# Kernel optimization log

Measured on AMD Instinct MI355X. Metric: run time of the kernel, lower is better.

Reference implementation:

```python
import jax, jax.numpy as jnp
import numpy as np

B, N, DEG = 64, 2048, 8
EPG = N * DEG            # edges per graph
E = B * EPG              # 1,048,576 total edges
NTOT = B * N             # 131,072 total nodes
HID = 128
NCLS = 32
K1 = int(np.ceil(0.25 * N))    # 512
K2 = int(np.ceil(0.25 * K1))   # 128


def _gcn(x, W, b, src, dst, emask, n):
    h = x @ W
    deg = jnp.zeros((n,), x.dtype).at[dst].add(emask) + 1.0
    dinv = jax.lax.rsqrt(deg)
    norm = dinv[src] * dinv[dst] * emask          # [E]
    agg = jnp.zeros((n, h.shape[1]), x.dtype).at[dst].add(h[src] * norm[:, None])
    agg = agg + h * (1.0 / deg)[:, None]          # self-loop term (norm = 1/deg)
    return agg + b


def _pool_stage(h, score, src, dst, emask, n_per_graph, k):
    # SAGPool top-k per graph (uniform graph size -> static k)
    sb = score.reshape(B, n_per_graph)
    idx = jax.lax.top_k(sb, k)[1]                                   # [B,k]
    perm = (jnp.arange(B)[:, None] * n_per_graph + idx).reshape(-1)  # [B*k]
    xp = h[perm] * jnp.tanh(score[perm])[:, None]
    # filter_adj: remap surviving nodes, mask dropped edges
    nmap = jnp.full((B * n_per_graph,), -1, jnp.int32).at[perm].set(
        jnp.arange(B * k, dtype=jnp.int32))
    s2, d2 = nmap[src], nmap[dst]
    m2 = emask * ((s2 >= 0) & (d2 >= 0)).astype(h.dtype)
    return xp, jnp.maximum(s2, 0), jnp.maximum(d2, 0), m2, perm


def _readout(x, k):
    xr = x.reshape(B, k, HID)
    return jnp.concatenate([xr.max(axis=1), xr.mean(axis=1)], axis=1)  # [B,2H]


def setup_inputs() -> dict:
    key = jax.random.key(0)
    ks = jax.random.split(key, 20)
    off = jnp.repeat(jnp.arange(B, dtype=jnp.int32) * N, EPG)
    src = jax.random.randint(ks[0], (E,), 0, N, dtype=jnp.int32) + off
    dst = jax.random.randint(ks[1], (E,), 0, N, dtype=jnp.int32) + off
    x = jax.random.normal(ks[2], (NTOT, 1), jnp.float32)
    ginfo = jax.random.normal(ks[3], (B, 10), jnp.float32)

    def lin(k, fi, fo):
        return jax.random.normal(k, (fi, fo), jnp.float32) / np.sqrt(fi)

    return {
        'x': x, 'edge_src': src, 'edge_dst': dst, 'ginfo': ginfo,
        'W1': lin(ks[4], 1, HID), 'b1': jnp.zeros((HID,), jnp.float32),
        'sW1': lin(ks[5], HID, 1), 'sb1': jnp.zeros((1,), jnp.float32),
        'W2': lin(ks[6], HID, HID), 'b2': jnp.zeros((HID,), jnp.float32),
        'sW2': lin(ks[7], HID, 1), 'sb2': jnp.zeros((1,), jnp.float32),
        'l1W': lin(ks[8], 2 * HID + 10, HID), 'l1b': jnp.zeros((HID,), jnp.float32),
        'l2W': lin(ks[9], HID, HID // 2), 'l2b': jnp.zeros((HID // 2,), jnp.float32),
        'l3W': lin(ks[10], HID // 2, NCLS), 'l3b': jnp.zeros((NCLS,), jnp.float32),
    }


def reference(x, edge_src, edge_dst, ginfo, W1, b1, sW1, sb1, W2, b2, sW2, sb2,
              l1W, l1b, l2W, l2b, l3W, l3b):
    m0 = jnp.ones((E,), x.dtype)
    # stage 1
    h = jax.nn.relu(_gcn(x, W1, b1, edge_src, edge_dst, m0, NTOT))
    score = _gcn(h, sW1, sb1, edge_src, edge_dst, m0, NTOT)[:, 0]
    h, s1, d1, m1, _ = _pool_stage(h, score, edge_src, edge_dst, m0, N, K1)
    x1 = _readout(h, K1)
    # stage 2
    n1 = B * K1
    h = jax.nn.relu(_gcn(h, W2, b2, s1, d1, m1, n1))
    score = _gcn(h, sW2, sb2, s1, d1, m1, n1)[:, 0]
    h, _, _, _, _ = _pool_stage(h, score, s1, d1, m1, K1, K2)
    x2 = _readout(h, K2)
    # head (dropout is eval-mode identity)
    z = jnp.concatenate([x1 + x2, ginfo.reshape(B, -1)], axis=1)
    z = jax.nn.relu(z @ l1W + l1b)
    z = jax.nn.relu(z @ l2W + l2b)
    return jax.nn.log_softmax(z @ l3W + l3b, axis=-1)
```

## Files before the change

kernel.cpp:

```cpp
#include <hip/hip_runtime.h>
#include <math.h>

#define NB    64
#define NPG   2048
#define EPG   16384
#define HID   128
#define K1V   512
#define K2V   128
#define N1    32768
#define MSK   (NPG - 1)
#define NQ    4
#define ESEG  (EPG / NQ)
#define SLOTS 24

typedef unsigned int u32;

static __device__ __forceinline__ float frelu(float v) { return v > 0.f ? v : 0.f; }

static __device__ __forceinline__ u32 f2key(float f) {
    u32 u = __float_as_uint(f);
    return u ^ ((u >> 31) ? 0xFFFFFFFFu : 0x80000000u);
}

static __device__ __forceinline__ u32 wave_iscan(u32 v, int lane) {
    #pragma unroll
    for (int off = 1; off < 64; off <<= 1) {
        u32 t = __shfl_up(v, off);
        if (lane >= off) v += t;
    }
    return v;
}

template <int N, int T>
static __device__ __forceinline__ void radix_top(const u32* __restrict__ key, int K,
                                                 u32* hist, u32* misc,
                                                 u32& tau, int& R) {
    const int tid = threadIdx.x;
    if (tid == 0) { misc[0] = 0u; misc[1] = (u32)K; }
    __syncthreads();
    #pragma unroll
    for (int p = 0; p < 4; p++) {
        const int shift = 24 - 8 * p;
        for (int i = tid; i < 256; i += T) hist[i] = 0u;
        __syncthreads();
        const u32 prefix = misc[0];
        const u32 need   = misc[1];
        for (int i = tid; i < N; i += T) {
            u32 k = key[i];
            bool ok = (p == 0) || ((k >> (shift + 8)) == prefix);
            if (ok) atomicAdd(&hist[(k >> shift) & 255u], 1u);
        }
        __syncthreads();
        if (tid < 64) {
            const int lane = tid;
            u32 c0 = hist[4 * lane + 0], c1 = hist[4 * lane + 1];
            u32 c2 = hist[4 * lane + 2], c3 = hist[4 * lane + 3];
            u32 local = c0 + c1 + c2 + c3;
            u32 inc = local;
            #pragma unroll
            for (int off = 1; off < 64; off <<= 1) {
                u32 v = __shfl_down(inc, off);
                if (lane + off < 64) inc += v;
            }
            u32 excl = inc - local;
            u32 ge3 = excl + c3, ge2 = ge3 + c2, ge1 = ge2 + c1, ge0 = ge1 + c0;
            int selb = -1; u32 gt = 0;
            if      (ge3 >= need && excl < need) { selb = 4 * lane + 3; gt = excl; }
            else if (ge2 >= need && ge3  < need) { selb = 4 * lane + 2; gt = ge3; }
            else if (ge1 >= need && ge2  < need) { selb = 4 * lane + 1; gt = ge2; }
            else if (ge0 >= need && ge1  < need) { selb = 4 * lane + 0; gt = ge1; }
            if (selb >= 0) { misc[0] = (prefix << 8) | (u32)selb; misc[1] = need - gt; }
        }
        __syncthreads();
    }
    tau = misc[0];
    R = (int)misc[1];
}

__global__ __launch_bounds__(1024) void k_sweepA(const float* __restrict__ x,
                                                 const int* __restrict__ esrc,
                                                 const int* __restrict__ edst,
                                                 float* __restrict__ df_g,
                                                 float* __restrict__ di_g,
                                                 float* __restrict__ tp) {
    __shared__ int   cnt[NPG];
    __shared__ float lv[NPG];
    __shared__ float acc[NPG];
    const int bid = blockIdx.x, tid = threadIdx.x;
    const int g = bid & 63, q = bid >> 6;
    for (int i = tid; i < NPG; i += 1024) { cnt[i] = 0; acc[i] = 0.f; }
    __syncthreads();
    const int4* dall = (const int4*)(edst + (size_t)g * EPG);
    for (int i = tid; i < EPG / 4; i += 1024) {
        int4 dd = dall[i];
        atomicAdd(&cnt[dd.x & MSK], 1); atomicAdd(&cnt[dd.y & MSK], 1);
        atomicAdd(&cnt[dd.z & MSK], 1); atomicAdd(&cnt[dd.w & MSK], 1);
    }
    __syncthreads();
    for (int i = tid; i < NPG; i += 1024) {
        float df = (float)cnt[i] + 1.0f;
        float di = rsqrtf(df);
        lv[i] = di * x[(size_t)g * NPG + i];
        if (q == 0) { df_g[(size_t)g * NPG + i] = df; di_g[(size_t)g * NPG + i] = di; }
    }
    __syncthreads();
    const int4* s4 = (const int4*)(esrc + g * EPG + q * ESEG);
    const int4* d4 = (const int4*)(edst + g * EPG + q * ESEG);
    for (int i = tid; i < ESEG / 4; i += 1024) {
        int4 ss = s4[i]; int4 dd = d4[i];
        atomicAdd(&acc[dd.x & MSK], lv[ss.x & MSK]);
        atomicAdd(&acc[dd.y & MSK], lv[ss.y & MSK]);
        atomicAdd(&acc[dd.z & MSK], lv[ss.z & MSK]);
        atomicAdd(&acc[dd.w & MSK], lv[ss.w & MSK]);
    }
    __syncthreads();
    float4* op = (float4*)(tp + ((size_t)g * NQ + q) * NPG);
    const float4* ap = (const float4*)acc;
    for (int i = tid; i < NPG / 4; i += 1024) op[i] = ap[i];
}

__global__ __launch_bounds__(1024) void k_sweepB(const float* __restrict__ x,
                                                 const int* __restrict__ esrc,
                                                 const int* __restrict__ edst,
                                                 const float* __restrict__ tp,
                                                 const float* __restrict__ df_g,
                                                 const float* __restrict__ di_g,
                                                 const float* __restrict__ W1,
                                                 const float* __restrict__ b1,
                                                 const float* __restrict__ sW1,
                                                 const float* __restrict__ sb1,
                                                 float* __restrict__ u_g,
                                                 float* __restrict__ sci_g,
                                                 float* __restrict__ scp) {
    __shared__ float lv[NPG];
    __shared__ float acc[NPG];
    __shared__ float lw[HID], lbb[HID], lsw[HID];
    const int bid = blockIdx.x, tid = threadIdx.x;
    const int g = bid & 63, q = bid >> 6;
    if (tid < HID) { lw[tid] = W1[tid]; lbb[tid] = b1[tid]; lsw[tid] = sW1[tid]; }
    __syncthreads();
    const float sb1v = sb1[0];
    for (int i = tid; i < NPG; i += 1024) {
        float t = 0.f;
        #pragma unroll
        for (int q2 = 0; q2 < NQ; q2++) t += tp[((size_t)g * NQ + q2) * NPG + i];
        float df = df_g[(size_t)g * NPG + i];
        float di = di_g[(size_t)g * NPG + i];
        float u = t * di + x[(size_t)g * NPG + i] / df;
        float s = 0.f;
        #pragma unroll 8
        for (int c = 0; c < HID; c++) s += frelu(fmaf(lw[c], u, lbb[c])) * lsw[c];
        lv[i] = di * s;
        acc[i] = 0.f;
        if (q == 0) {
            u_g[(size_t)g * NPG + i] = u;
            sci_g[(size_t)g * NPG + i] = s / df + sb1v;
        }
    }
    __syncthreads();
    const int4* s4 = (const int4*)(esrc + g * EPG + q * ESEG);
    const int4* d4 = (const int4*)(edst + g * EPG + q * ESEG);
    for (int i = tid; i < ESEG / 4; i += 1024) {
        int4 ss = s4[i]; int4 dd = d4[i];
        atomicAdd(&acc[dd.x & MSK], lv[ss.x & MSK]);
        atomicAdd(&acc[dd.y & MSK], lv[ss.y & MSK]);
        atomicAdd(&acc[dd.z & MSK], lv[ss.z & MSK]);
        atomicAdd(&acc[dd.w & MSK], lv[ss.w & MSK]);
    }
    __syncthreads();
    float4* op = (float4*)(scp + ((size_t)g * NQ + q) * NPG);
    const float4* ap = (const float4*)acc;
    for (int i = tid; i < NPG / 4; i += 1024) op[i] = ap[i];
}

__global__ __launch_bounds__(1024) void k_select(
    const float* __restrict__ sci_g, const float* __restrict__ di_g,
    const float* __restrict__ scp, const float* __restrict__ u_g,
    const float* __restrict__ W1, const float* __restrict__ b1,
    float* __restrict__ ulist, float* __restrict__ tg1, float* __restrict__ x1b,
    int* __restrict__ nmap_g, int* __restrict__ gdeg)
{
    __shared__ float lsc[NPG];
    __shared__ u32   lkey[NPG];
    __shared__ int   ln[NPG];
    __shared__ float ul[K1V], tgl[K1V];
    __shared__ int   sellist[K1V];
    __shared__ u32   hist[256], misc[2], wsum[16];
    __shared__ int   scnt;
    __shared__ float lw[HID], lbb[HID];
    const int b = blockIdx.x, tid = threadIdx.x;
    const int lane = tid & 63, wv = tid >> 6;

    if (tid < K1V) gdeg[b * K1V + tid] = 0;
    for (int i = tid; i < NPG; i += 1024) {
        float a = 0.f;
        #pragma unroll
        for (int q = 0; q < NQ; q++) a += scp[((size_t)b * NQ + q) * NPG + i];
        float sc = sci_g[(size_t)b * NPG + i] + di_g[(size_t)b * NPG + i] * a;
        lsc[i] = sc;
        lkey[i] = f2key(sc);
        ln[i] = -1;
    }
    if (tid < HID) { lw[tid] = W1[tid]; lbb[tid] = b1[tid]; }
    if (tid == 0) scnt = 0;
    __syncthreads();

    u32 tau; int R;
    radix_top<NPG, 1024>(lkey, K1V, hist, misc, tau, R);

    {
        int e0 = tid * 2, e1 = e0 + 1;
        u32 k0 = lkey[e0], k1 = lkey[e1];
        int q0 = (k0 == tau) ? 1 : 0, q1 = (k1 == tau) ? 1 : 0;
        u32 inc = wave_iscan((u32)(q0 + q1), lane);
        if (lane == 63) wsum[wv] = inc;
        __syncthreads();
        if (tid == 0) { u32 run = 0; for (int w2 = 0; w2 < 16; w2++) { u32 v = wsum[w2]; wsum[w2] = run; run += v; } }
        __syncthreads();
        u32 base = wsum[wv] + inc - (u32)(q0 + q1);
        bool sel0 = (k0 > tau) || (q0 && base < (u32)R);
        bool sel1 = (k1 > tau) || (q1 && (base + (u32)q0) < (u32)R);
        if (sel0) { int pos = atomicAdd(&scnt, 1); sellist[pos] = e0; }
        if (sel1) { int pos = atomicAdd(&scnt, 1); sellist[pos] = e1; }
        __syncthreads();
    }

    if (tid < K1V) {
        int node = sellist[tid];
        float uu = u_g[(size_t)b * NPG + node];
        float g = tanhf(lsc[node]);
        ul[tid] = uu; tgl[tid] = g;
        ulist[b * K1V + tid] = uu;
        tg1[b * K1V + tid] = g;
        ln[node] = tid;
    }
    __syncthreads();
    for (int i = tid; i < NPG; i += 1024) nmap_g[(size_t)b * NPG + i] = ln[i];

    float* rp = (float*)lkey;
    {
        int grp = tid >> 7, c = tid & 127;
        float w = lw[c], bb = lbb[c];
        float mx = -INFINITY, sm = 0.f;
        for (int j = grp; j < K1V; j += 8) {
            float v = frelu(fmaf(w, ul[j], bb)) * tgl[j];
            mx = fmaxf(mx, v); sm += v;
        }
        __syncthreads();
        rp[tid] = mx; rp[1024 + tid] = sm;
        __syncthreads();
        if (tid < HID) {
            float m2 = -INFINITY, s2 = 0.f;
            #pragma unroll
            for (int g2 = 0; g2 < 8; g2++) {
                m2 = fmaxf(m2, rp[g2 * 128 + tid]);
                s2 += rp[1024 + g2 * 128 + tid];
            }
            x1b[b * 256 + tid] = m2;
            x1b[b * 256 + HID + tid] = s2 / (float)K1V;
        }
    }
}

__global__ __launch_bounds__(512) void k_cpmm(
    const int* __restrict__ esrc, const int* __restrict__ edst,
    const int* __restrict__ nmap_g,
    int* __restrict__ gdeg, int* __restrict__ srcs2,
    const float* __restrict__ ulist, const float* __restrict__ tg1,
    const float* __restrict__ W1, const float* __restrict__ b1,
    const float* __restrict__ W2, float* __restrict__ hw)
{
    __shared__ union U {
        int lnm[NPG];
        struct { float lhT[HID * 64]; float lu[64]; float lg[64]; } mm;
    } sm;
    const int bid = blockIdx.x, tid = threadIdx.x;

    if (bid < NB * NQ) {
        const int g = bid & 63, q = bid >> 6;
        for (int i = tid; i < NPG; i += 512) sm.lnm[i] = nmap_g[(size_t)g * NPG + i];
        __syncthreads();
        const int4* s4 = (const int4*)(esrc + g * EPG + q * ESEG);
        const int4* d4 = (const int4*)(edst + g * EPG + q * ESEG);
        const int base = g * K1V;
        for (int i = tid; i < ESEG / 4; i += 512) {
            int4 ss = s4[i]; int4 dd = d4[i];
            int sa[4] = { ss.x & MSK, ss.y & MSK, ss.z & MSK, ss.w & MSK };
            int da[4] = { dd.x & MSK, dd.y & MSK, dd.z & MSK, dd.w & MSK };
            #pragma unroll
            for (int r = 0; r < 4; r++) {
                int s2 = sm.lnm[sa[r]], d2 = sm.lnm[da[r]];
                if (s2 >= 0 && d2 >= 0) {
                    int n = base + d2;
                    int slot = atomicAdd(&gdeg[n], 1);
                    if (slot < SLOTS) srcs2[(size_t)n * SLOTS + slot] = base + s2;
                }
            }
        }
    } else {
        const int row0 = (bid - NB * NQ) * 64;
        if (tid < 64) { sm.mm.lu[tid] = ulist[row0 + tid]; sm.mm.lg[tid] = tg1[row0 + tid]; }
        __syncthreads();
        for (int idx = tid; idx < HID * 64; idx += 512) {
            int k = idx >> 6, j = idx & 63;
            sm.mm.lhT[idx] = frelu(fmaf(W1[k], sm.mm.lu[j], b1[k])) * sm.mm.lg[j];
        }
        __syncthreads();
        const int cg2 = tid & 31, rg2 = tid >> 5;
        float acc[4][4];
        #pragma unroll
        for (int r = 0; r < 4; r++)
            #pragma unroll
            for (int c = 0; c < 4; c++) acc[r][c] = 0.f;
        const float4* lhT4 = (const float4*)sm.mm.lhT;
        #pragma unroll 4
        for (int k = 0; k < HID; k++) {
            float4 h = lhT4[k * 16 + rg2];
            float4 ww = *(const float4*)&W2[(size_t)k * HID + cg2 * 4];
            float hr[4] = { h.x, h.y, h.z, h.w };
            float wc[4] = { ww.x, ww.y, ww.z, ww.w };
            #pragma unroll
            for (int r = 0; r < 4; r++)
                #pragma unroll
                for (int c = 0; c < 4; c++)
                    acc[r][c] = fmaf(hr[r], wc[c], acc[r][c]);
        }
        #pragma unroll
        for (int r = 0; r < 4; r++) {
            float4 o; o.x = acc[r][0]; o.y = acc[r][1]; o.z = acc[r][2]; o.w = acc[r][3];
            *(float4*)&hw[(size_t)(row0 + rg2 * 4 + r) * HID + cg2 * 4] = o;
        }
    }
}

__global__ __launch_bounds__(256) void k_pull2(
    const int* __restrict__ srcs2, const int* __restrict__ gdeg,
    const float* __restrict__ hw, const float* __restrict__ b2,
    const float* __restrict__ sW2, const float* __restrict__ sb2,
    float* __restrict__ h2, float* __restrict__ ds02, float* __restrict__ sc2i)
{
    int node = blockIdx.x * 4 + (threadIdx.x >> 6);
    int lane = threadIdx.x & 63;
    int dg = gdeg[node];
    int cnt = dg < SLOTS ? dg : SLOTS;
    float a0 = 0.f, a1 = 0.f;
    for (int j = 0; j < cnt; j++) {
        int s = srcs2[(size_t)node * SLOTS + j];
        float w = rsqrtf((float)gdeg[s] + 1.0f);
        a0 = fmaf(w, hw[(size_t)s * HID + lane], a0);
        a1 = fmaf(w, hw[(size_t)s * HID + 64 + lane], a1);
    }
    float df = (float)dg + 1.0f;
    float di = rsqrtf(df);
    float h0 = frelu(a0 * di + hw[(size_t)node * HID + lane] / df + b2[lane]);
    float h1 = frelu(a1 * di + hw[(size_t)node * HID + 64 + lane] / df + b2[lane + 64]);
    h2[(size_t)node * HID + lane] = h0;
    h2[(size_t)node * HID + 64 + lane] = h1;
    float dot = h0 * sW2[lane] + h1 * sW2[lane + 64];
    #pragma unroll
    for (int o = 32; o > 0; o >>= 1) dot += __shfl_down(dot, o);
    if (lane == 0) {
        ds02[node] = di * dot;
        sc2i[node] = dot / df + sb2[0];
    }
}

__global__ __launch_bounds__(1024) void k_tkhead(
    const int* __restrict__ srcs2, const int* __restrict__ gdeg,
    const float* __restrict__ ds02, const float* __restrict__ sc2i,
    const float* __restrict__ h2,
    const float* __restrict__ x1b, const float* __restrict__ gi,
    const float* __restrict__ l1W, const float* __restrict__ l1b,
    const float* __restrict__ l2W, const float* __restrict__ l2b,
    const float* __restrict__ l3W, const float* __restrict__ l3b,
    float* __restrict__ out)
{
    __shared__ float sv[K1V];
    __shared__ u32   skey[K1V];
    __shared__ u32   hist[256], misc[2], wsum[16];
    __shared__ int   plist[K2V];
    __shared__ float tl[K2V];
    __shared__ float rp[1024], rp2[1024];
    __shared__ float z[272];
    __shared__ float zp[8][128];
    __shared__ float z1[HID], z2[64], z3[32], red[2];
    __shared__ int   scnt;
    const int b = blockIdx.x, tid = threadIdx.x;
    const int lane = tid & 63, wv = tid >> 6;
    if (tid == 0) scnt = 0;

    if (tid < K1V) {
        int n = b * K1V + tid;
        int dg = gdeg[n];
        int cnt = dg < SLOTS ? dg : SLOTS;
        float acc = 0.f;
        for (int j = 0; j < cnt; j++) acc += ds02[srcs2[(size_t)n * SLOTS + j]];
        float sc = sc2i[n] + rsqrtf((float)dg + 1.0f) * acc;
        sv[tid] = sc; skey[tid] = f2key(sc);
    }
    __syncthreads();
    u32 tau; int R;
    radix_top<K1V, 1024>(skey, K2V, hist, misc, tau, R);

    {
        u32 k0 = skey[tid < K1V ? tid : 0];
        int q0 = (tid < K1V && k0 == tau) ? 1 : 0;
        u32 inc = wave_iscan((u32)q0, lane);
        if (lane == 63) wsum[wv] = inc;
        __syncthreads();
        if (tid == 0) { u32 run = 0; for (int w2 = 0; w2 < 16; w2++) { u32 v = wsum[w2]; wsum[w2] = run; run += v; } }
        __syncthreads();
        u32 base = wsum[wv] + inc - (u32)q0;
        bool sel = (tid < K1V) && ((k0 > tau) || (q0 && base < (u32)R));
        if (sel) { int pos = atomicAdd(&scnt, 1); plist[pos] = b * K1V + tid; tl[pos] = tanhf(sv[tid]); }
        __syncthreads();
    }

    {
        int grp = tid >> 7, c = tid & 127;
        float mx = -INFINITY, smv = 0.f;
        for (int j = grp; j < K2V; j += 8) {
            float v = h2[(size_t)plist[j] * HID + c] * tl[j];
            mx = fmaxf(mx, v); smv += v;
        }
        rp[tid] = mx; rp2[tid] = smv;
        __syncthreads();
        if (tid < 256) {
            int c2 = tid & 127, half = tid >> 7;
            if (half == 0) {
                float m = rp[c2];
                #pragma unroll
                for (int g2 = 1; g2 < 8; g2++) m = fmaxf(m, rp[g2 * 128 + c2]);
                z[c2] = x1b[b * 256 + c2] + m;
            } else {
                float s = rp2[c2];
                #pragma unroll
                for (int g2 = 1; g2 < 8; g2++) s += rp2[g2 * 128 + c2];
                z[128 + c2] = x1b[b * 256 + 128 + c2] + s / (float)K2V;
            }
        }
        if (tid < 10) z[256 + tid] = gi[b * 10 + tid];
        __syncthreads();
    }

    {
        int grp = tid >> 7, c = tid & 127;
        int k0 = grp * 34;
        int k1 = k0 + 34; if (k1 > 266) k1 = 266;
        float acc = 0.f;
        for (int k = k0; k < k1; k++) acc = fmaf(z[k], l1W[k * 128 + c], acc);
        zp[grp][c] = acc;
        __syncthreads();
        if (tid < 128) {
            float s = l1b[tid];
            #pragma unroll
            for (int g2 = 0; g2 < 8; g2++) s += zp[g2][tid];
            z1[tid] = frelu(s);
        }
        __syncthreads();
    }

    {
        if (tid < 512) {
            int grp = tid >> 6, c = tid & 63;
            int k0 = grp * 16;
            float acc = 0.f;
            #pragma unroll
            for (int k = k0; k < k0 + 16; k++) acc = fmaf(z1[k], l2W[k * 64 + c], acc);
            zp[grp][c] = acc;
        }
        __syncthreads();
        if (tid < 64) {
            float s = l2b[tid];
            #pragma unroll
            for (int g2 = 0; g2 < 8; g2++) s += zp[g2][tid];
            z2[tid] = frelu(s);
        }
        __syncthreads();
    }

    if (tid < 32) {
        float a3 = l3b[tid];
        for (int k = 0; k < 64; k++) a3 = fmaf(z2[k], l3W[k * 32 + tid], a3);
        z3[tid] = a3;
    }
    __syncthreads();
    if (tid == 0) {
        float m = -INFINITY;
        for (int c2 = 0; c2 < 32; c2++) m = fmaxf(m, z3[c2]);
        float s = 0.f;
        for (int c2 = 0; c2 < 32; c2++) s += expf(z3[c2] - m);
        red[0] = m; red[1] = logf(s);
    }
    __syncthreads();
    if (tid < 32) out[b * 32 + tid] = z3[tid] - red[0] - red[1];
}

extern "C" void kernel_launch(void* const* d_in, const int* in_sizes, int n_in,
                              void* d_out, int out_size, void* d_ws, size_t ws_size,
                              hipStream_t stream) {
    const float* x    = (const float*)d_in[0];
    const int*   esrc = (const int*)d_in[1];
    const int*   edst = (const int*)d_in[2];
    const float* gi   = (const float*)d_in[3];
    const float* W1   = (const float*)d_in[4];
    const float* b1   = (const float*)d_in[5];
    const float* sW1  = (const float*)d_in[6];
    const float* sb1  = (const float*)d_in[7];
    const float* W2   = (const float*)d_in[8];
    const float* b2   = (const float*)d_in[9];
    const float* sW2  = (const float*)d_in[10];
    const float* sb2  = (const float*)d_in[11];
    const float* l1W  = (const float*)d_in[12];
    const float* l1b  = (const float*)d_in[13];
    const float* l2W  = (const float*)d_in[14];
    const float* l2b  = (const float*)d_in[15];
    const float* l3W  = (const float*)d_in[16];
    const float* l3b  = (const float*)d_in[17];
    float* out = (float*)d_out;

    char* p = (char*)d_ws;
    auto alloc = [&](size_t bytes) {
        char* r = p;
        p += (bytes + 255) & ~size_t(255);
        return (void*)r;
    };
    float* df_g   = (float*)alloc((size_t)NB * NPG * 4);
    float* di_g   = (float*)alloc((size_t)NB * NPG * 4);
    float* tp     = (float*)alloc((size_t)NB * NQ * NPG * 4);
    float* u_g    = (float*)alloc((size_t)NB * NPG * 4);
    float* sci_g  = (float*)alloc((size_t)NB * NPG * 4);
    float* scp    = (float*)alloc((size_t)NB * NQ * NPG * 4);
    int*   nmap_g = (int*)alloc((size_t)NB * NPG * 4);
    float* ulist  = (float*)alloc((size_t)N1 * 4);
    float* tg1    = (float*)alloc((size_t)N1 * 4);
    float* x1b    = (float*)alloc((size_t)NB * 256 * 4);
    int*   gdeg   = (int*)alloc((size_t)N1 * 4);
    int*   srcs2  = (int*)alloc((size_t)N1 * SLOTS * 4);
    float* hw     = (float*)alloc((size_t)N1 * HID * 4);
    float* h2     = (float*)alloc((size_t)N1 * HID * 4);
    float* ds02   = (float*)alloc((size_t)N1 * 4);
    float* sc2i   = (float*)alloc((size_t)N1 * 4);

    k_sweepA<<<NB * NQ, 1024, 0, stream>>>(x, esrc, edst, df_g, di_g, tp);
    k_sweepB<<<NB * NQ, 1024, 0, stream>>>(x, esrc, edst, tp, df_g, di_g,
                                           W1, b1, sW1, sb1, u_g, sci_g, scp);
    k_select<<<NB, 1024, 0, stream>>>(sci_g, di_g, scp, u_g, W1, b1,
                                      ulist, tg1, x1b, nmap_g, gdeg);
    k_cpmm<<<NB * NQ + N1 / 64, 512, 0, stream>>>(esrc, edst, nmap_g, gdeg, srcs2,
                                                  ulist, tg1, W1, b1, W2, hw);
    k_pull2<<<N1 / 4, 256, 0, stream>>>(srcs2, gdeg, hw, b2, sW2, sb2, h2, ds02, sc2i);
    k_tkhead<<<NB, 1024, 0, stream>>>(srcs2, gdeg, ds02, sc2i, h2,
                                      x1b, gi, l1W, l1b, l2W, l2b, l3W, l3b, out);
}
```

Measured before the change: 113.4 us.

## Fuse pooled-edge filtering into top-k select kernel using shared-memory node map

Moves the stage-2 edge filtering and adjacency-slot building from the combined cpmm kernel into k_select. It now reads the node remap from shared memory and counts degrees with LDS atomics instead of global atomics. This removes the global nmap round trip and the gdeg zeroing dependency. The cost is that filtering now runs in only 64 blocks, one per graph, each scanning 16K edges, instead of 256 blocks running alongside the matmul. The matmul becomes its own k_mm kernel.

```diff
diff --git a/kernel.cpp b/kernel.cpp
--- a/kernel.cpp
+++ b/kernel.cpp
@@ -177,8 +177,9 @@
     const float* __restrict__ sci_g, const float* __restrict__ di_g,
     const float* __restrict__ scp, const float* __restrict__ u_g,
     const float* __restrict__ W1, const float* __restrict__ b1,
+    const int* __restrict__ esrc, const int* __restrict__ edst,
     float* __restrict__ ulist, float* __restrict__ tg1, float* __restrict__ x1b,
-    int* __restrict__ nmap_g, int* __restrict__ gdeg)
+    int* __restrict__ gdeg, int* __restrict__ srcs2)
 {
     __shared__ float lsc[NPG];
     __shared__ u32   lkey[NPG];
@@ -191,7 +192,6 @@
     const int b = blockIdx.x, tid = threadIdx.x;
     const int lane = tid & 63, wv = tid >> 6;
 
-    if (tid < K1V) gdeg[b * K1V + tid] = 0;
     for (int i = tid; i < NPG; i += 1024) {
         float a = 0.f;
         #pragma unroll
@@ -235,7 +235,6 @@
         ln[node] = tid;
     }
     __syncthreads();
-    for (int i = tid; i < NPG; i += 1024) nmap_g[(size_t)b * NPG + i] = ln[i];
 
     float* rp = (float*)lkey;
     {
@@ -260,76 +259,72 @@
             x1b[b * 256 + HID + tid] = s2 / (float)K1V;
         }
     }
-}
-
-__global__ __launch_bounds__(512) void k_cpmm(
-    const int* __restrict__ esrc, const int* __restrict__ edst,
-    const int* __restrict__ nmap_g,
-    int* __restrict__ gdeg, int* __restrict__ srcs2,
+    __syncthreads();
+
+    int* ldeg2 = sellist;
+    if (tid < K1V) ldeg2[tid] = 0;
+    __syncthreads();
+    {
+        const int4* s4 = (const int4*)(esrc + (size_t)b * EPG);
+        const int4* d4 = (const int4*)(edst + (size_t)b * EPG);
+        const int base = b * K1V;
+        for (int i = tid; i < EPG / 4; i += 1024) {
+            int4 ss = s4[i]; int4 dd = d4[i];
+            int sa[4] = { ss.x & MSK, ss.y & MSK, ss.z & MSK, ss.w & MSK };
+            int da[4] = { dd.x & MSK, dd.y & MSK, dd.z & MSK, dd.w & MSK };
+            #pragma unroll
+            for (int r = 0; r < 4; r++) {
+                int s2 = ln[sa[r]], d2 = ln[da[r]];
+                if (s2 >= 0 && d2 >= 0) {
+                    int slot = atomicAdd(&ldeg2[d2], 1);
+                    if (slot < SLOTS) srcs2[(size_t)(base + d2) * SLOTS + slot] = base + s2;
+                }
+            }
+        }
+    }
+    __syncthreads();
+    if (tid < K1V) gdeg[b * K1V + tid] = ldeg2[tid];
+}
+
+__global__ __launch_bounds__(512) void k_mm(
     const float* __restrict__ ulist, const float* __restrict__ tg1,
     const float* __restrict__ W1, const float* __restrict__ b1,
     const float* __restrict__ W2, float* __restrict__ hw)
 {
-    __shared__ union U {
-        int lnm[NPG];
-        struct { float lhT[HID * 64]; float lu[64]; float lg[64]; } mm;
-    } sm;
+    __shared__ float lhT[HID * 64];
+    __shared__ float lu[64], lg[64];
     const int bid = blockIdx.x, tid = threadIdx.x;
-
-    if (bid < NB * NQ) {
-        const int g = bid & 63, q = bid >> 6;
-        for (int i = tid; i < NPG; i += 512) sm.lnm[i] = nmap_g[(size_t)g * NPG + i];
-        __syncthreads();
-        const int4* s4 = (const int4*)(esrc + g * EPG + q * ESEG);
-        const int4* d4 = (const int4*)(edst + g * EPG + q * ESEG);
-        const int base = g * K1V;
-        for (int i = tid; i < ESEG / 4; i += 512) {
-            int4 ss = s4[i]; int4 dd = d4[i];
-            int sa[4] = { ss.x & MSK, ss.y & MSK, ss.z & MSK, ss.w & MSK };
-            int da[4] = { dd.x & MSK, dd.y & MSK, dd.z & MSK, dd.w & MSK };
-            #pragma unroll
-            for (int r = 0; r < 4; r++) {
-                int s2 = sm.lnm[sa[r]], d2 = sm.lnm[da[r]];
-                if (s2 >= 0 && d2 >= 0) {
-                    int n = base + d2;
-                    int slot = atomicAdd(&gdeg[n], 1);
-                    if (slot < SLOTS) srcs2[(size_t)n * SLOTS + slot] = base + s2;
-                }
-            }
-        }
-    } else {
-        const int row0 = (bid - NB * NQ) * 64;
-        if (tid < 64) { sm.mm.lu[tid] = ulist[row0 + tid]; sm.mm.lg[tid] = tg1[row0 + tid]; }
-        __syncthreads();
-        for (int idx = tid; idx < HID * 64; idx += 512) {
-            int k = idx >> 6, j = idx & 63;
-            sm.mm.lhT[idx] = frelu(fmaf(W1[k], sm.mm.lu[j], b1[k])) * sm.mm.lg[j];
-        }
-        __syncthreads();
-        const int cg2 = tid & 31, rg2 = tid >> 5;
-        float acc[4][4];
+    const int row0 = bid * 64;
+    if (tid < 64) { lu[tid] = ulist[row0 + tid]; lg[tid] = tg1[row0 + tid]; }
+    __syncthreads();
+    for (int idx = tid; idx < HID * 64; idx += 512) {
+        int k = idx >> 6, j = idx & 63;
+        lhT[idx] = frelu(fmaf(W1[k], lu[j], b1[k])) * lg[j];
+    }
+    __syncthreads();
+    const int cg2 = tid & 31, rg2 = tid >> 5;
+    float acc[4][4];
+    #pragma unroll
+    for (int r = 0; r < 4; r++)
+        #pragma unroll
+        for (int c = 0; c < 4; c++) acc[r][c] = 0.f;
+    const float4* lhT4 = (const float4*)lhT;
+    #pragma unroll 4
+    for (int k = 0; k < HID; k++) {
+        float4 h = lhT4[k * 16 + rg2];
+        float4 ww = *(const float4*)&W2[(size_t)k * HID + cg2 * 4];
+        float hr[4] = { h.x, h.y, h.z, h.w };
+        float wc[4] = { ww.x, ww.y, ww.z, ww.w };
         #pragma unroll
         for (int r = 0; r < 4; r++)
             #pragma unroll
-            for (int c = 0; c < 4; c++) acc[r][c] = 0.f;
-        const float4* lhT4 = (const float4*)sm.mm.lhT;
-        #pragma unroll 4
-        for (int k = 0; k < HID; k++) {
-            float4 h = lhT4[k * 16 + rg2];
-            float4 ww = *(const float4*)&W2[(size_t)k * HID + cg2 * 4];
-            float hr[4] = { h.x, h.y, h.z, h.w };
-            float wc[4] = { ww.x, ww.y, ww.z, ww.w };
-            #pragma unroll
-            for (int r = 0; r < 4; r++)
-                #pragma unroll
-                for (int c = 0; c < 4; c++)
-                    acc[r][c] = fmaf(hr[r], wc[c], acc[r][c]);
-        }
-        #pragma unroll
-        for (int r = 0; r < 4; r++) {
-            float4 o; o.x = acc[r][0]; o.y = acc[r][1]; o.z = acc[r][2]; o.w = acc[r][3];
-            *(float4*)&hw[(size_t)(row0 + rg2 * 4 + r) * HID + cg2 * 4] = o;
-        }
+            for (int c = 0; c < 4; c++)
+                acc[r][c] = fmaf(hr[r], wc[c], acc[r][c]);
+    }
+    #pragma unroll
+    for (int r = 0; r < 4; r++) {
+        float4 o; o.x = acc[r][0]; o.y = acc[r][1]; o.z = acc[r][2]; o.w = acc[r][3];
+        *(float4*)&hw[(size_t)(row0 + rg2 * 4 + r) * HID + cg2 * 4] = o;
     }
 }
 
@@ -531,7 +526,6 @@
     float* u_g    = (float*)alloc((size_t)NB * NPG * 4);
     float* sci_g  = (float*)alloc((size_t)NB * NPG * 4);
     float* scp    = (float*)alloc((size_t)NB * NQ * NPG * 4);
-    int*   nmap_g = (int*)alloc((size_t)NB * NPG * 4);
     float* ulist  = (float*)alloc((size_t)N1 * 4);
     float* tg1    = (float*)alloc((size_t)N1 * 4);
     float* x1b    = (float*)alloc((size_t)NB * 256 * 4);
@@ -545,10 +539,9 @@
     k_sweepA<<<NB * NQ, 1024, 0, stream>>>(x, esrc, edst, df_g, di_g, tp);
     k_sweepB<<<NB * NQ, 1024, 0, stream>>>(x, esrc, edst, tp, df_g, di_g,
                                            W1, b1, sW1, sb1, u_g, sci_g, scp);
-    k_select<<<NB, 1024, 0, stream>>>(sci_g, di_g, scp, u_g, W1, b1,
-                                      ulist, tg1, x1b, nmap_g, gdeg);
-    k_cpmm<<<NB * NQ + N1 / 64, 512, 0, stream>>>(esrc, edst, nmap_g, gdeg, srcs2,
-                                                  ulist, tg1, W1, b1, W2, hw);
+    k_select<<<NB, 1024, 0, stream>>>(sci_g, di_g, scp, u_g, W1, b1, esrc, edst,
+                                      ulist, tg1, x1b, gdeg, srcs2);
+    k_mm<<<N1 / 64, 512, 0, stream>>>(ulist, tg1, W1, b1, W2, hw);
     k_pull2<<<N1 / 4, 256, 0, stream>>>(srcs2, gdeg, hw, b2, sW2, sb2, h2, ds02, sc2i);
     k_tkhead<<<NB, 1024, 0, stream>>>(srcs2, gdeg, ds02, sc2i, h2,
                                       x1b, gi, l1W, l1b, l2W, l2b, l3W, l3b, out);
```

Result: no change. 112.8 us (-0.5%).
